# Optimization experiments

Hardware: AMD Instinct MI355X
Metric: run time of the kernel (lower is better)

## Reference

```python
import jax, jax.numpy as jnp
import numpy as np

# Graph / model dims (match init_kwargs config)
N1, N2, N3 = 80000, 16000, 4096
E1, E2 = 256000, 65536
D_IN, H1, C1 = 256, 8, 64   # conv1: concat -> 512
H2, C2 = 4, 64              # conv2: mean over heads -> gnn_outdim=64
F_IN, F_HID, L_DIM, N_CLS = 128, 64, 64, 1


def setup_inputs() -> dict:
    key = jax.random.key(0)
    ks = jax.random.split(key, 20)
    rng = np.random.default_rng(0)

    def edges(E, n_src, n_dst):
        src = rng.integers(0, n_src, size=E)
        dst = rng.integers(0, n_dst, size=E)
        # avoid incidental self loops (PyG remove_self_loops); explicit ones added in conv
        src = np.where(src == dst, src + 1, src)
        return jnp.asarray(src, jnp.int32), jnp.asarray(dst, jnp.int32)

    es1, ed1 = edges(E1, N1, N2)
    es2, ed2 = edges(E2, N2, N3)
    s = 0.05
    return {
        "x": jax.random.normal(ks[0], (N1, D_IN), jnp.float32),
        "flat": jax.random.normal(ks[1], (N3, F_IN), jnp.float32),
        "last": jax.random.normal(ks[2], (N3, L_DIM), jnp.float32),
        "edge_src1": es1, "edge_dst1": ed1,
        "edge_src2": es2, "edge_dst2": ed2,
        "W1_src": jax.random.normal(ks[3], (D_IN, H1 * C1), jnp.float32) * s,
        "W1_dst": jax.random.normal(ks[4], (D_IN, H1 * C1), jnp.float32) * s,
        "att1_src": jax.random.normal(ks[5], (H1, C1), jnp.float32) * s,
        "att1_dst": jax.random.normal(ks[6], (H1, C1), jnp.float32) * s,
        "bias1": jax.random.normal(ks[7], (H1 * C1,), jnp.float32) * s,
        "W2_src": jax.random.normal(ks[8], (H1 * C1, H2 * C2), jnp.float32) * s,
        "W2_dst": jax.random.normal(ks[9], (H1 * C1, H2 * C2), jnp.float32) * s,
        "att2_src": jax.random.normal(ks[10], (H2, C2), jnp.float32) * s,
        "att2_dst": jax.random.normal(ks[11], (H2, C2), jnp.float32) * s,
        "bias2": jax.random.normal(ks[12], (C2,), jnp.float32) * s,
        "flat_W": jax.random.normal(ks[13], (F_IN, F_HID), jnp.float32) * s,
        "flat_b": jax.random.normal(ks[14], (F_HID,), jnp.float32) * s,
        "out_W": jax.random.normal(ks[15], (C2 + F_HID + L_DIM, N_CLS), jnp.float32) * s,
        "out_b": jax.random.normal(ks[16], (N_CLS,), jnp.float32) * s,
    }


def gat_conv(x_src, x_dst, src, dst, W_s, W_d, a_s, a_d, b, concat):
    """PyG bipartite GATConv (eval mode, add_self_loops=True, neg slope 0.2)."""
    H, C = a_s.shape
    Ns, Nd = x_src.shape[0], x_dst.shape[0]
    h_s = (x_src @ W_s).reshape(Ns, H, C)
    h_d = (x_dst @ W_d).reshape(Nd, H, C)
    sl = jnp.arange(Nd, dtype=src.dtype)
    src = jnp.concatenate([src, sl])  # self loops on target nodes
    dst = jnp.concatenate([dst, sl])
    e_s = jnp.einsum("nhc,hc->nh", h_s, a_s)  # [Ns,H]
    e_d = jnp.einsum("nhc,hc->nh", h_d, a_d)  # [Nd,H]
    alpha = jax.nn.leaky_relu(e_s[src] + e_d[dst], negative_slope=0.2)  # [E,H]
    amax = jax.ops.segment_max(alpha, dst, num_segments=Nd)[dst]
    ex = jnp.exp(alpha - amax)
    w = ex / jax.ops.segment_sum(ex, dst, num_segments=Nd)[dst]  # segment softmax
    msg = w[:, :, None] * h_s[src]  # [E,H,C]
    out = jax.ops.segment_sum(msg, dst, num_segments=Nd)  # [Nd,H,C]
    out = out.reshape(Nd, H * C) if concat else out.mean(axis=1)
    return out + b


def reference(x, flat, last, edge_src1, edge_dst1, edge_src2, edge_dst2,
              W1_src, W1_dst, att1_src, att1_dst, bias1,
              W2_src, W2_dst, att2_src, att2_dst, bias2,
              flat_W, flat_b, out_W, out_b):
    # eval mode: featdrop / attndrop / main_dropout are identity
    h = gat_conv(x, x[:N2], edge_src1, edge_dst1,
                 W1_src, W1_dst, att1_src, att1_dst, bias1, concat=True)
    h = jax.nn.elu(h)
    h = gat_conv(h, h[:N3], edge_src2, edge_dst2,
                 W2_src, W2_dst, att2_src, att2_dst, bias2, concat=False)
    f = flat @ flat_W + flat_b
    z = jnp.concatenate([h, f, last], axis=1)  # [N3, 64+64+64]
    return z @ out_W + out_b  # [N3, num_cls]
```

## Files before the change

### kernel.cpp

```cpp
#include <hip/hip_runtime.h>
#include <hip/hip_bf16.h>
#include <cstdio>

typedef __attribute__((ext_vector_type(8))) short short8;
typedef __attribute__((ext_vector_type(4))) short short4v;
typedef __attribute__((ext_vector_type(8))) _Float16 half8;
typedef __attribute__((ext_vector_type(4))) float f32x4;

template <int H> struct VecT;
template <> struct VecT<8> { using T = short8; };
template <> struct VecT<4> { using T = short4v; };

__device__ __forceinline__ float bfu2f(unsigned short u) {
    return __uint_as_float(((unsigned)u) << 16);
}
__device__ __forceinline__ unsigned short f2bfu(float f) {
    __hip_bfloat16 b = __float2bfloat16(f);
    union { __hip_bfloat16 b; unsigned short u; } cv; cv.b = b;
    return cv.u;
}
__device__ __forceinline__ unsigned short f2hu(float f) {
    _Float16 h = (_Float16)f;
    union { _Float16 h; unsigned short u; } cv; cv.h = h;
    return cv.u;
}

#define N1 80000
#define N2 16000
#define N3 4096
#define E1 256000
#define E2 65536

__global__ void prep_kernel(const float* __restrict__ W1s, const float* __restrict__ W1d,
                            unsigned short* __restrict__ w1s_pk, unsigned short* __restrict__ w1d_pk,
                            const float* __restrict__ W2s, const float* __restrict__ W2d,
                            unsigned short* __restrict__ w2s_pk, unsigned short* __restrict__ w2d_pk,
                            const float* __restrict__ fW, unsigned short* __restrict__ fw_t3,
                            int* __restrict__ zbase, int zn) {
    int i = blockIdx.x * blockDim.x + threadIdx.x;
    const int S0 = 262144, S1 = 262144, S2 = 8192;
    if (i < S0) {
        const float* W = (i < 131072) ? W1s : W1d;
        unsigned short* pk = (i < 131072) ? w1s_pk : w1d_pk;
        int j = i & 131071;
        int k = j >> 9, n = j & 511;
        int n16 = n >> 4, l = n & 15, k32 = k >> 5, qq = (k >> 3) & 3, e = k & 7;
        size_t base = ((size_t)(n16 * 8 + k32)) * 512 + (qq * 16 + l) * 8 + e;
        pk[base] = f2hu(W[j]);
    } else if (i < S0 + S1) {
        int ii = i - S0;
        const float* W = (ii < 131072) ? W2s : W2d;
        unsigned short* pk = (ii < 131072) ? w2s_pk : w2d_pk;
        int j = ii & 131071;
        int k = j >> 8, n = j & 255;
        int n16 = n >> 4, l = n & 15, k32 = k >> 5, qq = (k >> 3) & 3, e = k & 7;
        size_t base = ((size_t)(n16 * 16 + k32)) * 512 + (qq * 16 + l) * 8 + e;
        pk[base] = f2hu(W[j]);
    } else if (i < S0 + S1 + S2) {
        int j = i - S0 - S1;
        int k = j >> 6, n = j & 63;
        float v = fW[j];
        unsigned short h = f2bfu(v);
        unsigned short l = f2bfu(v - bfu2f(h));
        size_t base = (size_t)n * 384;
        fw_t3[base + k] = h;
        fw_t3[base + 128 + k] = l;
        fw_t3[base + 256 + k] = h;
    } else {
        int j = i - S0 - S1 - S2;
        if (j < zn) zbase[j] = 0;
    }
}

__global__ void hist_dual(const int* __restrict__ d1, int* __restrict__ c1,
                          const int* __restrict__ d2, int* __restrict__ c2) {
    int i = blockIdx.x * blockDim.x + threadIdx.x;
    if (i < E1) {
        int d = d1[i];
        if ((unsigned)d < (unsigned)N2) atomicAdd(&c1[d], 1);
    } else if (i < E1 + E2) {
        int d = d2[i - E1];
        if ((unsigned)d < (unsigned)N3) atomicAdd(&c2[d], 1);
    }
}
__global__ __launch_bounds__(1024)
void scan_dual(const int* __restrict__ c1, int* __restrict__ s1, int Nd1,
               const int* __restrict__ c2, int* __restrict__ s2, int Nd2) {
    const int* cnt = (blockIdx.x == 0) ? c1 : c2;
    int* start = (blockIdx.x == 0) ? s1 : s2;
    int Nd = (blockIdx.x == 0) ? Nd1 : Nd2;
    __shared__ int part[1024];
    int t = threadIdx.x;
    int k = (Nd + 1023) >> 10;
    int lo = t * k, hi = min(lo + k, Nd);
    if (lo > Nd) lo = Nd;
    int s = 0;
    for (int i = lo; i < hi; i++) s += cnt[i];
    part[t] = s;
    __syncthreads();
    for (int off = 1; off < 1024; off <<= 1) {
        int v = (t >= off) ? part[t - off] : 0;
        __syncthreads();
        part[t] += v;
        __syncthreads();
    }
    int run = (t > 0) ? part[t - 1] : 0;
    for (int i = lo; i < hi; i++) { start[i] = run; run += cnt[i]; }
    if (t == 1023) start[Nd] = part[1023];
}
__global__ void fill_dual(const int* __restrict__ sa1, const int* __restrict__ da1,
                          const int* __restrict__ st1, int* __restrict__ cu1, int* __restrict__ cs1,
                          const int* __restrict__ sa2, const int* __restrict__ da2,
                          const int* __restrict__ st2, int* __restrict__ cu2, int* __restrict__ cs2) {
    int i = blockIdx.x * blockDim.x + threadIdx.x;
    const int *sa, *da, *st;
    int *cu, *cs;
    int Nd, Ns, e;
    if (i < E1) { sa = sa1; da = da1; st = st1; cu = cu1; cs = cs1; Nd = N2; Ns = N1; e = i; }
    else if (i < E1 + E2) { sa = sa2; da = da2; st = st2; cu = cu2; cs = cs2; Nd = N3; Ns = N2; e = i - E1; }
    else return;
    int d = da[e];
    if ((unsigned)d >= (unsigned)Nd) return;
    int p = atomicAdd(&cu[d], 1);
    int idx = st[d] + p;
    if (idx >= st[d + 1]) return;
    int s = sa[e];
    if ((unsigned)s >= (unsigned)Ns) s = 0;
    cs[idx] = s;
}

template <bool AF16>
__global__ __launch_bounds__(256, 2)
void gemm_lds(const void* __restrict__ Ax,
              const unsigned short* __restrict__ Bp1, unsigned short* __restrict__ C1,
              const float* __restrict__ att1, float* __restrict__ es1,
              const unsigned short* __restrict__ Bp2, unsigned short* __restrict__ C2,
              const float* __restrict__ att2, float* __restrict__ es2,
              int Mb1, int MT, int NB, int N, int K, int H) {
    __shared__ alignas(16) _Float16 As[2][64][72];
    const int hb = blockIdx.x;
    const int xcd = hb & 7;
    const int sI = hb >> 3;
    const int mt = (sI / NB) * 8 + xcd;
    const int nb = sI % NB;
    if (mt >= MT) return;
    const unsigned short* Bp; unsigned short* C; const float* att; float* es_out;
    int m0;
    if (mt < Mb1) { Bp = Bp1; C = C1; att = att1; es_out = es1; m0 = mt * 64; }
    else          { Bp = Bp2; C = C2; att = att2; es_out = es2; m0 = (mt - Mb1) * 64; }
    const int tid = threadIdx.x;
    const int wave = tid >> 6, lane = tid & 63;
    const int q = lane >> 4, l15 = lane & 15;
    const int n0 = nb * 256 + wave * 64;
    const int KS = K >> 6;
    const int KSB = K >> 5;
    const int arow = tid >> 2, ac16 = (tid & 3) * 16;
    const unsigned short* Bbase = Bp + (size_t)(n0 >> 4) * KSB * 512 + lane * 8;

    f32x4 acc[4][4] = {};
    half8 b[2][4];
    float4 s0, s1, s2, s3;
    half8 sh0, sh1;

    auto stageLoad = [&](int t) {
        if constexpr (AF16) {
            const _Float16* p = (const _Float16*)Ax + (size_t)(m0 + arow) * K + t * 64 + ac16;
            sh0 = *(const half8*)p;
            sh1 = *(const half8*)(p + 8);
        } else {
            const float* p = (const float*)Ax + (size_t)(m0 + arow) * K + t * 64 + ac16;
            s0 = *(const float4*)p;
            s1 = *(const float4*)(p + 4);
            s2 = *(const float4*)(p + 8);
            s3 = *(const float4*)(p + 12);
        }
    };
    auto stageWrite = [&](int buf) {
        half8 v0, v1;
        if constexpr (AF16) {
            v0 = sh0; v1 = sh1;
        } else {
            v0[0] = (_Float16)s0.x; v0[1] = (_Float16)s0.y;
            v0[2] = (_Float16)s0.z; v0[3] = (_Float16)s0.w;
            v0[4] = (_Float16)s1.x; v0[5] = (_Float16)s1.y;
            v0[6] = (_Float16)s1.z; v0[7] = (_Float16)s1.w;
            v1[0] = (_Float16)s2.x; v1[1] = (_Float16)s2.y;
            v1[2] = (_Float16)s2.z; v1[3] = (_Float16)s2.w;
            v1[4] = (_Float16)s3.x; v1[5] = (_Float16)s3.y;
            v1[6] = (_Float16)s3.z; v1[7] = (_Float16)s3.w;
        }
        *(half8*)&As[buf][arow][ac16] = v0;
        *(half8*)&As[buf][arow][ac16 + 8] = v1;
    };
    auto loadB = [&](int k32, int kh, int nt) {
        b[kh][nt] = *(const half8*)(Bbase + ((size_t)nt * KSB + k32) * 512);
    };

    stageLoad(0);
#pragma unroll
    for (int kh = 0; kh < 2; kh++)
#pragma unroll
        for (int nt = 0; nt < 4; nt++) loadB(kh, kh, nt);
    stageWrite(0);
    __syncthreads();

    int cur = 0;
    for (int t = 0; t < KS; t++) {
        const bool hn = (t + 1) < KS;
        if (hn) stageLoad(t + 1);
#pragma unroll
        for (int kh = 0; kh < 2; kh++) {
#pragma unroll
            for (int rg = 0; rg < 4; rg++) {
                half8 a = *(const half8*)&As[cur][rg * 16 + l15][kh * 32 + q * 8];
#pragma unroll
                for (int nt = 0; nt < 4; nt++) {
                    acc[rg][nt] = __builtin_amdgcn_mfma_f32_16x16x32_f16(a, b[kh][nt], acc[rg][nt], 0, 0, 0);
                    if (rg == 3 && hn) loadB(2 * (t + 1) + kh, kh, nt);
                }
            }
        }
        if (hn) {
            stageWrite(cur ^ 1);
            __syncthreads();
        }
        cur ^= 1;
    }

#pragma unroll
    for (int rg = 0; rg < 4; rg++)
#pragma unroll
        for (int nt = 0; nt < 4; nt++)
#pragma unroll
            for (int r = 0; r < 4; r++) {
                int row = m0 + rg * 16 + q * 4 + r;
                int col = n0 + nt * 16 + l15;
                C[(size_t)row * N + col] = f2bfu(acc[rg][nt][r]);
            }
    {
        const int head = n0 >> 6;
        float av[4];
#pragma unroll
        for (int nt = 0; nt < 4; nt++) av[nt] = att[head * 64 + nt * 16 + l15];
#pragma unroll
        for (int rg = 0; rg < 4; rg++)
#pragma unroll
            for (int r = 0; r < 4; r++) {
                float p = acc[rg][0][r] * av[0] + acc[rg][1][r] * av[1]
                        + acc[rg][2][r] * av[2] + acc[rg][3][r] * av[3];
#pragma unroll
                for (int off = 1; off < 16; off <<= 1) p += __shfl_xor(p, off);
                if (l15 == 0)
                    es_out[(size_t)(m0 + rg * 16 + q * 4 + r) * H + head] = p;
            }
    }
}

__global__ __launch_bounds__(256)
void gemm_mfma(const float* __restrict__ A, const unsigned short* __restrict__ Bt3,
               float* __restrict__ C, int M, int N, int K) {
    const int KK = 3 * K;
    __shared__ unsigned short As[2][64][72];
    __shared__ unsigned short Bs[64][72];
    const int tid = threadIdx.x;
    const int wave = tid >> 6, lane = tid & 63;
    const int wr = wave >> 1, wc = wave & 1;
    const int quad = lane >> 4, l15 = lane & 15;
    const int m0 = blockIdx.y * 64, n0 = blockIdx.x * 64;
    f32x4 acc[2][2] = {};
    for (int k0 = 0; k0 < KK; k0 += 64) {
        const int seg = k0 / K;
        const int ks = k0 - seg * K;
#pragma unroll
        for (int i = 0; i < 2; i++) {
            int idx = tid + i * 256;
            int r = idx >> 3, cv = (idx & 7) * 8;
            const float* ap = &A[(size_t)(m0 + r) * K + ks + cv];
            const float4 v0 = *(const float4*)ap;
            const float4 v1 = *(const float4*)(ap + 4);
            float va[8] = {v0.x, v0.y, v0.z, v0.w, v1.x, v1.y, v1.z, v1.w};
            short8 h8, l8;
#pragma unroll
            for (int j = 0; j < 8; j++) {
                unsigned short hh = f2bfu(va[j]);
                h8[j] = (short)hh;
                l8[j] = (short)f2bfu(va[j] - bfu2f(hh));
            }
            *(short8*)&As[0][r][cv] = h8;
            *(short8*)&As[1][r][cv] = l8;
            *(short8*)&Bs[r][cv] = *(const short8*)&Bt3[(size_t)(n0 + r) * KK + k0 + cv];
        }
        __syncthreads();
        const int abank = (seg < 2) ? 0 : 1;
#pragma unroll
        for (int kk = 0; kk < 64; kk += 32) {
            short8 a[2], b[2];
#pragma unroll
            for (int t = 0; t < 2; t++) {
                a[t] = *(const short8*)&As[abank][wr * 32 + t * 16 + l15][kk + quad * 8];
                b[t] = *(const short8*)&Bs[wc * 32 + t * 16 + l15][kk + quad * 8];
            }
#pragma unroll
            for (int mt = 0; mt < 2; mt++)
#pragma unroll
                for (int nt = 0; nt < 2; nt++)
                    acc[mt][nt] = __builtin_amdgcn_mfma_f32_16x16x32_bf16(
                        a[mt], b[nt], acc[mt][nt], 0, 0, 0);
        }
        __syncthreads();
    }
#pragma unroll
    for (int mt = 0; mt < 2; mt++)
#pragma unroll
        for (int nt = 0; nt < 2; nt++)
#pragma unroll
            for (int r = 0; r < 4; r++) {
                int row = m0 + wr * 32 + mt * 16 + quad * 4 + r;
                int col = n0 + wc * 32 + nt * 16 + l15;
                C[(size_t)row * N + col] = acc[mt][nt][r];
            }
}

template <int H, bool ELU, bool HOUT>
__global__ __launch_bounds__(256)
void gat_agg2(const int* __restrict__ csr, const int* __restrict__ rs,
              const unsigned short* __restrict__ hs,
              const float* __restrict__ es,
              const float* __restrict__ ed,
              const float* __restrict__ bias,
              void* __restrict__ out,
              int Nd) {
    constexpr int LH = (H == 8) ? 3 : 2;
    constexpr int EPC = 64 >> LH;
    const int lane = threadIdx.x & 63;
    const int d = blockIdx.x * (blockDim.x >> 6) + (threadIdx.x >> 6);
    if (d >= Nd) return;
    const int beg = rs[d];
    const int deg = rs[d + 1] - beg;
    const int n = deg + 1;
    const int h = lane & (H - 1);
    const int e0 = lane >> LH;
    const float edh = ed[(size_t)d * H + h];
    const int nch = (n + EPC - 1) / EPC;
    float mx = -1e30f;
    float den = 0.0f;
    if (nch <= 8) {
        float ac[8];
#pragma unroll
        for (int c = 0; c < 8; c++) {
            float a = -1e30f;
            if (c < nch) {
                int j = c * EPC + e0;
                if (j < n) {
                    int s = (j < deg) ? csr[beg + j] : d;
                    a = es[(size_t)s * H + h] + edh;
                    a = (a > 0.0f) ? a : 0.2f * a;
                }
            }
            ac[c] = a;
            mx = fmaxf(mx, a);
        }
#pragma unroll
        for (int off = H; off < 64; off <<= 1) mx = fmaxf(mx, __shfl_xor(mx, off));
#pragma unroll
        for (int c = 0; c < 8; c++)
            if (c < nch) den += expf(ac[c] - mx);
#pragma unroll
        for (int off = H; off < 64; off <<= 1) den += __shfl_xor(den, off);
    } else {
        for (int j0 = 0; j0 < n; j0 += EPC) {
            int j = j0 + e0;
            if (j < n) {
                int s = (j < deg) ? csr[beg + j] : d;
                float a = es[(size_t)s * H + h] + edh;
                a = (a > 0.0f) ? a : 0.2f * a;
                mx = fmaxf(mx, a);
            }
        }
#pragma unroll
        for (int off = H; off < 64; off <<= 1) mx = fmaxf(mx, __shfl_xor(mx, off));
        for (int j0 = 0; j0 < n; j0 += EPC) {
            int j = j0 + e0;
            if (j < n) {
                int s = (j < deg) ? csr[beg + j] : d;
                float a = es[(size_t)s * H + h] + edh;
                a = (a > 0.0f) ? a : 0.2f * a;
                den += expf(a - mx);
            }
        }
#pragma unroll
        for (int off = H; off < 64; off <<= 1) den += __shfl_xor(den, off);
    }
    const float inv = 1.0f / den;
    const int hB = lane >> (6 - LH);
    const float mB = __shfl(mx, hB);
    const float invB = __shfl(inv, hB);
    const float edhB = __shfl(edh, hB);
    using V = typename VecT<H>::T;
    float acc[H] = {};
    const size_t rowoff = (size_t)lane * H;
    int j = 0;
    for (; j + 8 <= n; j += 8) {
        int s[8]; V rv[8]; float w[8];
#pragma unroll
        for (int u = 0; u < 8; u++) { int jj = j + u; s[u] = (jj < deg) ? csr[beg + jj] : d; }
#pragma unroll
        for (int u = 0; u < 8; u++) rv[u] = *(const V*)&hs[(size_t)s[u] * (H * 64) + rowoff];
#pragma unroll
        for (int u = 0; u < 8; u++) {
            float a = es[(size_t)s[u] * H + hB] + edhB;
            a = (a > 0.0f) ? a : 0.2f * a;
            w[u] = expf(a - mB) * invB;
        }
#pragma unroll
        for (int u = 0; u < 8; u++)
#pragma unroll
            for (int k = 0; k < H; k++) acc[k] += w[u] * bfu2f((unsigned short)rv[u][k]);
    }
    for (; j + 4 <= n; j += 4) {
        int s[4]; V rv[4]; float w[4];
#pragma unroll
        for (int u = 0; u < 4; u++) { int jj = j + u; s[u] = (jj < deg) ? csr[beg + jj] : d; }
#pragma unroll
        for (int u = 0; u < 4; u++) rv[u] = *(const V*)&hs[(size_t)s[u] * (H * 64) + rowoff];
#pragma unroll
        for (int u = 0; u < 4; u++) {
            float a = es[(size_t)s[u] * H + hB] + edhB;
            a = (a > 0.0f) ? a : 0.2f * a;
            w[u] = expf(a - mB) * invB;
        }
#pragma unroll
        for (int u = 0; u < 4; u++)
#pragma unroll
            for (int k = 0; k < H; k++) acc[k] += w[u] * bfu2f((unsigned short)rv[u][k]);
    }
    for (; j < n; j++) {
        int s = (j < deg) ? csr[beg + j] : d;
        V rv = *(const V*)&hs[(size_t)s * (H * 64) + rowoff];
        float a = es[(size_t)s * H + hB] + edhB;
        a = (a > 0.0f) ? a : 0.2f * a;
        float w = expf(a - mB) * invB;
#pragma unroll
        for (int k = 0; k < H; k++) acc[k] += w * bfu2f((unsigned short)rv[k]);
    }
#pragma unroll
    for (int k = 0; k < H; k++) {
        float v = acc[k];
        if (ELU) {
            v += bias[lane * H + k];
            v = (v > 0.0f) ? v : expm1f(v);
        }
        acc[k] = v;
    }
    if constexpr (HOUT) {
        half8 hv;
#pragma unroll
        for (int k = 0; k < H; k++) hv[k] = (_Float16)acc[k];
        _Float16* op = (_Float16*)out + (size_t)d * (H * 64) + rowoff;
        *(half8*)op = hv;
    } else {
        float* op = (float*)out + (size_t)d * (H * 64) + rowoff;
#pragma unroll
        for (int qd = 0; qd < H / 4; qd++)
            *(float4*)&op[qd * 4] = *(float4*)&acc[qd * 4];
    }
}

__global__ void final_kernel(const float* __restrict__ acc2, const float* __restrict__ bias2,
                             const float* __restrict__ fbuf, const float* __restrict__ flat_b,
                             const float* __restrict__ last, const float* __restrict__ outW,
                             const float* __restrict__ outb, float* __restrict__ out, int N) {
    int n = blockIdx.x * blockDim.x + threadIdx.x;
    if (n >= N) return;
    float s = outb[0];
    const float* a = acc2 + (size_t)n * 256;
    for (int c = 0; c < 64; c++) {
        float h2 = 0.25f * (a[c] + a[64 + c] + a[128 + c] + a[192 + c]) + bias2[c];
        s += h2 * outW[c];
        s += (fbuf[(size_t)n * 64 + c] + flat_b[c]) * outW[64 + c];
        s += last[(size_t)n * 64 + c] * outW[128 + c];
    }
    out[n] = s;
}

extern "C" void kernel_launch(void* const* d_in, const int* in_sizes, int n_in,
                              void* d_out, int out_size, void* d_ws, size_t ws_size,
                              hipStream_t stream) {
    const float* x    = (const float*)d_in[0];
    const float* flat = (const float*)d_in[1];
    const float* last = (const float*)d_in[2];
    const int*  es1i  = (const int*)d_in[3];
    const int*  ed1i  = (const int*)d_in[4];
    const int*  es2i  = (const int*)d_in[5];
    const int*  ed2i  = (const int*)d_in[6];
    const float* W1s  = (const float*)d_in[7];
    const float* W1d  = (const float*)d_in[8];
    const float* a1s  = (const float*)d_in[9];
    const float* a1d  = (const float*)d_in[10];
    const float* b1   = (const float*)d_in[11];
    const float* W2s  = (const float*)d_in[12];
    const float* W2d  = (const float*)d_in[13];
    const float* a2s  = (const float*)d_in[14];
    const float* a2d  = (const float*)d_in[15];
    const float* b2   = (const float*)d_in[16];
    const float* fW   = (const float*)d_in[17];
    const float* fb   = (const float*)d_in[18];
    const float* oW   = (const float*)d_in[19];
    const float* ob   = (const float*)d_in[20];
    float* out = (float*)d_out;

    float* ws = (float*)d_ws;
    unsigned short* hs1_bf = (unsigned short*)ws;
    unsigned short* hd1_bf = (unsigned short*)(ws + 20480000);
    float* es1f = ws + 24576000;
    float* ed1f = ws + 25216000;
    float* acc1 = ws + 25344000;
    unsigned short* wb = (unsigned short*)(ws + 54016000);
    unsigned short* w1s_pk = wb;
    unsigned short* w1d_pk = wb + 262144;
    unsigned short* w2s_pk = wb + 524288;
    unsigned short* w2d_pk = wb + 786432;
    unsigned short* fw_t3  = wb + 1048576;
    int* ibase   = (int*)(ws + 54816000);
    int* cnt1    = ibase;
    int* cursor1 = ibase + 16000;
    int* cnt2    = ibase + 32000;
    int* cursor2 = ibase + 36096;
    int* start1  = ibase + 40192;
    int* start2  = ibase + 56193;
    int* csr1    = ibase + 60290;
    int* csr2    = ibase + 316290;
    const size_t NEED = ((size_t)54816000 + 381826) * 4;
    if (ws_size < NEED) {
        fprintf(stderr, "kernel_launch: ws_size %zu < needed %zu\n", ws_size, NEED);
        return;
    }
    unsigned short* hs2_bf = (unsigned short*)ws;
    unsigned short* hd2_bf = (unsigned short*)(ws + 2048000);
    float* es2f = ws + 2572288;
    float* ed2f = ws + 2636288;
    float* acc2 = ws + 2652672;
    float* fbuf = ws + 3701248;
    unsigned short* acc1h = (unsigned short*)acc1;

    {
        int total = 262144 + 262144 + 8192 + 40192;
        prep_kernel<<<(total + 255) / 256, 256, 0, stream>>>(
            W1s, W1d, w1s_pk, w1d_pk,
            W2s, W2d, w2s_pk, w2d_pk,
            fW, fw_t3, ibase, 40192);
    }
    hist_dual<<<(E1 + E2 + 255) / 256, 256, 0, stream>>>(ed1i, cnt1, ed2i, cnt2);
    scan_dual<<<2, 1024, 0, stream>>>(cnt1, start1, N2, cnt2, start2, N3);
    fill_dual<<<(E1 + E2 + 255) / 256, 256, 0, stream>>>(
        es1i, ed1i, start1, cursor1, csr1, es2i, ed2i, start2, cursor2, csr2);

    {
        const int MT = N1 / 64 + N2 / 64;
        const int NB = 512 / 256;
        const int grid = 8 * NB * ((MT + 7) / 8);
        gemm_lds<false><<<grid, 256, 0, stream>>>(
            x, w1s_pk, hs1_bf, a1s, es1f,
            w1d_pk, hd1_bf, a1d, ed1f,
            N1 / 64, MT, NB, 512, 256, 8);
    }
    gat_agg2<8, true, true><<<N2 / 4, 256, 0, stream>>>(
        csr1, start1, hs1_bf, es1f, ed1f, b1, acc1h, N2);

    {
        const int MT = N2 / 64 + N3 / 64;
        const int NB = 1;
        const int grid = 8 * NB * ((MT + 7) / 8);
        gemm_lds<true><<<grid, 256, 0, stream>>>(
            acc1h, w2s_pk, hs2_bf, a2s, es2f,
            w2d_pk, hd2_bf, a2d, ed2f,
            N2 / 64, MT, NB, 256, 512, 4);
    }
    gat_agg2<4, false, false><<<N3 / 4, 256, 0, stream>>>(
        csr2, start2, hs2_bf, es2f, ed2f, nullptr, acc2, N3);

    gemm_mfma<<<dim3(1, N3 / 64), 256, 0, stream>>>(flat, fw_t3, fbuf, N3, 64, 128);
    final_kernel<<<(N3 + 255) / 256, 256, 0, stream>>>(acc2, b2, fbuf, fb, last, oW, ob, out, N3);
}
```

Before: 379.2 us.

## Fold destination attention into precomputed W_dst·a_dst vectors, drop dst GEMMs

The destination-side projection GEMM is no longer computed. Its only use was the attention logit e_d, so W_dst·att_dst is precomputed per head in the prep kernel and e_d is taken as a dot product of the raw destination features inside the aggregation kernel. This removes the N2 and N3 dst tiles from both GEMM launches and the hd buffers. The aggregation kernel also now reuses the cached per-chunk softmax exponentials in the low-degree path instead of recomputing es lookups and exp per edge. The cost is extra per-node dot-product work in aggregation and a small serial loop in prep, plus a reassociation of the fp math for e_d.

```diff
diff --git a/kernel.cpp b/kernel.cpp
--- a/kernel.cpp
+++ b/kernel.cpp
@@ -31,31 +31,27 @@
 #define E1 256000
 #define E2 65536
 
-__global__ void prep_kernel(const float* __restrict__ W1s, const float* __restrict__ W1d,
-                            unsigned short* __restrict__ w1s_pk, unsigned short* __restrict__ w1d_pk,
-                            const float* __restrict__ W2s, const float* __restrict__ W2d,
-                            unsigned short* __restrict__ w2s_pk, unsigned short* __restrict__ w2d_pk,
+__global__ void prep_kernel(const float* __restrict__ W1s, unsigned short* __restrict__ w1s_pk,
+                            const float* __restrict__ W2s, unsigned short* __restrict__ w2s_pk,
+                            const float* __restrict__ W1d, const float* __restrict__ a1d,
+                            float* __restrict__ v1dT,
+                            const float* __restrict__ W2d, const float* __restrict__ a2d,
+                            float* __restrict__ v2dT,
                             const float* __restrict__ fW, unsigned short* __restrict__ fw_t3,
                             int* __restrict__ zbase, int zn) {
     int i = blockIdx.x * blockDim.x + threadIdx.x;
-    const int S0 = 262144, S1 = 262144, S2 = 8192;
+    const int S0 = 131072, S1 = 131072, S2 = 8192, S3 = 4096;
     if (i < S0) {
-        const float* W = (i < 131072) ? W1s : W1d;
-        unsigned short* pk = (i < 131072) ? w1s_pk : w1d_pk;
-        int j = i & 131071;
-        int k = j >> 9, n = j & 511;
+        int k = i >> 9, n = i & 511;
         int n16 = n >> 4, l = n & 15, k32 = k >> 5, qq = (k >> 3) & 3, e = k & 7;
         size_t base = ((size_t)(n16 * 8 + k32)) * 512 + (qq * 16 + l) * 8 + e;
-        pk[base] = f2hu(W[j]);
+        w1s_pk[base] = f2hu(W1s[i]);
     } else if (i < S0 + S1) {
-        int ii = i - S0;
-        const float* W = (ii < 131072) ? W2s : W2d;
-        unsigned short* pk = (ii < 131072) ? w2s_pk : w2d_pk;
-        int j = ii & 131071;
+        int j = i - S0;
         int k = j >> 8, n = j & 255;
         int n16 = n >> 4, l = n & 15, k32 = k >> 5, qq = (k >> 3) & 3, e = k & 7;
         size_t base = ((size_t)(n16 * 16 + k32)) * 512 + (qq * 16 + l) * 8 + e;
-        pk[base] = f2hu(W[j]);
+        w2s_pk[base] = f2hu(W2s[j]);
     } else if (i < S0 + S1 + S2) {
         int j = i - S0 - S1;
         int k = j >> 6, n = j & 63;
@@ -66,8 +62,22 @@
         fw_t3[base + k] = h;
         fw_t3[base + 128 + k] = l;
         fw_t3[base + 256 + k] = h;
+    } else if (i < S0 + S1 + S2 + S3) {
+        int j = i - S0 - S1 - S2;
+        if (j < 2048) {
+            int h = j >> 8, k = j & 255;
+            float s = 0.f;
+            for (int c = 0; c < 64; c++) s += W1d[k * 512 + h * 64 + c] * a1d[h * 64 + c];
+            v1dT[j] = s;
+        } else {
+            int jj = j - 2048;
+            int h = jj >> 9, k = jj & 511;
+            float s = 0.f;
+            for (int c = 0; c < 64; c++) s += W2d[k * 256 + h * 64 + c] * a2d[h * 64 + c];
+            v2dT[jj] = s;
+        }
     } else {
-        int j = i - S0 - S1 - S2;
+        int j = i - S0 - S1 - S2 - S3;
         if (j < zn) zbase[j] = 0;
     }
 }
@@ -132,11 +142,9 @@
 template <bool AF16>
 __global__ __launch_bounds__(256, 2)
 void gemm_lds(const void* __restrict__ Ax,
-              const unsigned short* __restrict__ Bp1, unsigned short* __restrict__ C1,
-              const float* __restrict__ att1, float* __restrict__ es1,
-              const unsigned short* __restrict__ Bp2, unsigned short* __restrict__ C2,
-              const float* __restrict__ att2, float* __restrict__ es2,
-              int Mb1, int MT, int NB, int N, int K, int H) {
+              const unsigned short* __restrict__ Bp, unsigned short* __restrict__ C,
+              const float* __restrict__ att, float* __restrict__ es_out,
+              int MT, int NB, int N, int K, int H) {
     __shared__ alignas(16) _Float16 As[2][64][72];
     const int hb = blockIdx.x;
     const int xcd = hb & 7;
@@ -144,10 +152,7 @@
     const int mt = (sI / NB) * 8 + xcd;
     const int nb = sI % NB;
     if (mt >= MT) return;
-    const unsigned short* Bp; unsigned short* C; const float* att; float* es_out;
-    int m0;
-    if (mt < Mb1) { Bp = Bp1; C = C1; att = att1; es_out = es1; m0 = mt * 64; }
-    else          { Bp = Bp2; C = C2; att = att2; es_out = es2; m0 = (mt - Mb1) * 64; }
+    const int m0 = mt * 64;
     const int tid = threadIdx.x;
     const int wave = tid >> 6, lane = tid & 63;
     const int q = lane >> 4, l15 = lane & 15;
@@ -321,31 +326,58 @@
             }
 }
 
-template <int H, bool ELU, bool HOUT>
+template <int H, bool ELU, bool HOUT, bool XF16, int KD>
 __global__ __launch_bounds__(256)
 void gat_agg2(const int* __restrict__ csr, const int* __restrict__ rs,
               const unsigned short* __restrict__ hs,
               const float* __restrict__ es,
-              const float* __restrict__ ed,
+              const void* __restrict__ xsrc,
+              const float* __restrict__ vdT,
               const float* __restrict__ bias,
               void* __restrict__ out,
               int Nd) {
     constexpr int LH = (H == 8) ? 3 : 2;
     constexpr int EPC = 64 >> LH;
+    constexpr int KPL = KD / EPC;
     const int lane = threadIdx.x & 63;
     const int d = blockIdx.x * (blockDim.x >> 6) + (threadIdx.x >> 6);
     if (d >= Nd) return;
+    const int h = lane & (H - 1);
+    const int e0 = lane >> LH;
+    float edh = 0.f;
+    {
+        const float* vp = vdT + h * KD + e0 * KPL;
+        if constexpr (XF16) {
+            const _Float16* xr = (const _Float16*)xsrc + (size_t)d * KD + e0 * KPL;
+#pragma unroll
+            for (int i8 = 0; i8 < KPL / 8; i8++) {
+                half8 hx = *(const half8*)(xr + i8 * 8);
+#pragma unroll
+                for (int jj = 0; jj < 8; jj++) edh += (float)hx[jj] * vp[i8 * 8 + jj];
+            }
+        } else {
+            const float* xr = (const float*)xsrc + (size_t)d * KD + e0 * KPL;
+#pragma unroll
+            for (int i4 = 0; i4 < KPL / 4; i4++) {
+                float4 xv = *(const float4*)(xr + i4 * 4);
+                float4 vv = *(const float4*)(vp + i4 * 4);
+                edh += xv.x * vv.x + xv.y * vv.y + xv.z * vv.z + xv.w * vv.w;
+            }
+        }
+#pragma unroll
+        for (int off = H; off < 64; off <<= 1) edh += __shfl_xor(edh, off);
+    }
     const int beg = rs[d];
     const int deg = rs[d + 1] - beg;
     const int n = deg + 1;
-    const int h = lane & (H - 1);
-    const int e0 = lane >> LH;
-    const float edh = ed[(size_t)d * H + h];
     const int nch = (n + EPC - 1) / EPC;
-    float mx = -1e30f;
-    float den = 0.0f;
+    const int hB = lane >> (6 - LH);
+    using V = typename VecT<H>::T;
+    float acc[H] = {};
+    const size_t rowoff = (size_t)lane * H;
     if (nch <= 8) {
         float ac[8];
+        float mx = -1e30f;
 #pragma unroll
         for (int c = 0; c < 8; c++) {
             float a = -1e30f;
@@ -362,12 +394,38 @@
         }
 #pragma unroll
         for (int off = H; off < 64; off <<= 1) mx = fmaxf(mx, __shfl_xor(mx, off));
+        float den = 0.0f;
 #pragma unroll
         for (int c = 0; c < 8; c++)
             if (c < nch) den += expf(ac[c] - mx);
 #pragma unroll
         for (int off = H; off < 64; off <<= 1) den += __shfl_xor(den, off);
+        const float inv = 1.0f / den;
+        float ec[8];
+#pragma unroll
+        for (int c = 0; c < 8; c++) ec[c] = expf(ac[c] - mx) * inv;
+#pragma unroll
+        for (int c = 0; c < 8; c++) {
+            if (c >= nch) break;
+            const int jb = c * EPC;
+            const int cnt = min(EPC, n - jb);
+            int s[EPC]; V rv[EPC];
+#pragma unroll
+            for (int u = 0; u < EPC; u++)
+                if (u < cnt) { int jj = jb + u; s[u] = (jj < deg) ? csr[beg + jj] : d; }
+#pragma unroll
+            for (int u = 0; u < EPC; u++)
+                if (u < cnt) rv[u] = *(const V*)&hs[(size_t)s[u] * (H * 64) + rowoff];
+#pragma unroll
+            for (int u = 0; u < EPC; u++)
+                if (u < cnt) {
+                    float w = __shfl(ec[c], u * H + hB);
+#pragma unroll
+                    for (int k = 0; k < H; k++) acc[k] += w * bfu2f((unsigned short)rv[u][k]);
+                }
+        }
     } else {
+        float mx = -1e30f;
         for (int j0 = 0; j0 < n; j0 += EPC) {
             int j = j0 + e0;
             if (j < n) {
@@ -379,6 +437,7 @@
         }
 #pragma unroll
         for (int off = H; off < 64; off <<= 1) mx = fmaxf(mx, __shfl_xor(mx, off));
+        float den = 0.0f;
         for (int j0 = 0; j0 < n; j0 += EPC) {
             int j = j0 + e0;
             if (j < n) {
@@ -390,58 +449,37 @@
         }
 #pragma unroll
         for (int off = H; off < 64; off <<= 1) den += __shfl_xor(den, off);
-    }
-    const float inv = 1.0f / den;
-    const int hB = lane >> (6 - LH);
-    const float mB = __shfl(mx, hB);
-    const float invB = __shfl(inv, hB);
-    const float edhB = __shfl(edh, hB);
-    using V = typename VecT<H>::T;
-    float acc[H] = {};
-    const size_t rowoff = (size_t)lane * H;
-    int j = 0;
-    for (; j + 8 <= n; j += 8) {
-        int s[8]; V rv[8]; float w[8];
-#pragma unroll
-        for (int u = 0; u < 8; u++) { int jj = j + u; s[u] = (jj < deg) ? csr[beg + jj] : d; }
-#pragma unroll
-        for (int u = 0; u < 8; u++) rv[u] = *(const V*)&hs[(size_t)s[u] * (H * 64) + rowoff];
-#pragma unroll
-        for (int u = 0; u < 8; u++) {
-            float a = es[(size_t)s[u] * H + hB] + edhB;
+        const float inv = 1.0f / den;
+        const float mB = __shfl(mx, hB);
+        const float invB = __shfl(inv, hB);
+        const float edhB = __shfl(edh, hB);
+        int j = 0;
+        for (; j + 4 <= n; j += 4) {
+            int s[4]; V rv[4]; float w[4];
+#pragma unroll
+            for (int u = 0; u < 4; u++) { int jj = j + u; s[u] = (jj < deg) ? csr[beg + jj] : d; }
+#pragma unroll
+            for (int u = 0; u < 4; u++) rv[u] = *(const V*)&hs[(size_t)s[u] * (H * 64) + rowoff];
+#pragma unroll
+            for (int u = 0; u < 4; u++) {
+                float a = es[(size_t)s[u] * H + hB] + edhB;
+                a = (a > 0.0f) ? a : 0.2f * a;
+                w[u] = expf(a - mB) * invB;
+            }
+#pragma unroll
+            for (int u = 0; u < 4; u++)
+#pragma unroll
+                for (int k = 0; k < H; k++) acc[k] += w[u] * bfu2f((unsigned short)rv[u][k]);
+        }
+        for (; j < n; j++) {
+            int s = (j < deg) ? csr[beg + j] : d;
+            V rv = *(const V*)&hs[(size_t)s * (H * 64) + rowoff];
+            float a = es[(size_t)s * H + hB] + edhB;
             a = (a > 0.0f) ? a : 0.2f * a;
-            w[u] = expf(a - mB) * invB;
-        }
-#pragma unroll
-        for (int u = 0; u < 8; u++)
-#pragma unroll
-            for (int k = 0; k < H; k++) acc[k] += w[u] * bfu2f((unsigned short)rv[u][k]);
-    }
-    for (; j + 4 <= n; j += 4) {
-        int s[4]; V rv[4]; float w[4];
-#pragma unroll
-        for (int u = 0; u < 4; u++) { int jj = j + u; s[u] = (jj < deg) ? csr[beg + jj] : d; }
-#pragma unroll
-        for (int u = 0; u < 4; u++) rv[u] = *(const V*)&hs[(size_t)s[u] * (H * 64) + rowoff];
-#pragma unroll
-        for (int u = 0; u < 4; u++) {
-            float a = es[(size_t)s[u] * H + hB] + edhB;
-            a = (a > 0.0f) ? a : 0.2f * a;
-            w[u] = expf(a - mB) * invB;
-        }
-#pragma unroll
-        for (int u = 0; u < 4; u++)
-#pragma unroll
-            for (int k = 0; k < H; k++) acc[k] += w[u] * bfu2f((unsigned short)rv[u][k]);
-    }
-    for (; j < n; j++) {
-        int s = (j < deg) ? csr[beg + j] : d;
-        V rv = *(const V*)&hs[(size_t)s * (H * 64) + rowoff];
-        float a = es[(size_t)s * H + hB] + edhB;
-        a = (a > 0.0f) ? a : 0.2f * a;
-        float w = expf(a - mB) * invB;
-#pragma unroll
-        for (int k = 0; k < H; k++) acc[k] += w * bfu2f((unsigned short)rv[k]);
+            float w = expf(a - mB) * invB;
+#pragma unroll
+            for (int k = 0; k < H; k++) acc[k] += w * bfu2f((unsigned short)rv[k]);
+        }
     }
 #pragma unroll
     for (int k = 0; k < H; k++) {
@@ -511,16 +549,14 @@
 
     float* ws = (float*)d_ws;
     unsigned short* hs1_bf = (unsigned short*)ws;
-    unsigned short* hd1_bf = (unsigned short*)(ws + 20480000);
     float* es1f = ws + 24576000;
-    float* ed1f = ws + 25216000;
     float* acc1 = ws + 25344000;
     unsigned short* wb = (unsigned short*)(ws + 54016000);
     unsigned short* w1s_pk = wb;
-    unsigned short* w1d_pk = wb + 262144;
     unsigned short* w2s_pk = wb + 524288;
-    unsigned short* w2d_pk = wb + 786432;
     unsigned short* fw_t3  = wb + 1048576;
+    float* v1dT = ws + 54600000;
+    float* v2dT = ws + 54602048;
     int* ibase   = (int*)(ws + 54816000);
     int* cnt1    = ibase;
     int* cursor1 = ibase + 16000;
@@ -536,18 +572,16 @@
         return;
     }
     unsigned short* hs2_bf = (unsigned short*)ws;
-    unsigned short* hd2_bf = (unsigned short*)(ws + 2048000);
     float* es2f = ws + 2572288;
-    float* ed2f = ws + 2636288;
     float* acc2 = ws + 2652672;
     float* fbuf = ws + 3701248;
     unsigned short* acc1h = (unsigned short*)acc1;
 
     {
-        int total = 262144 + 262144 + 8192 + 40192;
+        int total = 131072 + 131072 + 8192 + 4096 + 40192;
         prep_kernel<<<(total + 255) / 256, 256, 0, stream>>>(
-            W1s, W1d, w1s_pk, w1d_pk,
-            W2s, W2d, w2s_pk, w2d_pk,
+            W1s, w1s_pk, W2s, w2s_pk,
+            W1d, a1d, v1dT, W2d, a2d, v2dT,
             fW, fw_t3, ibase, 40192);
     }
     hist_dual<<<(E1 + E2 + 255) / 256, 256, 0, stream>>>(ed1i, cnt1, ed2i, cnt2);
@@ -556,28 +590,23 @@
         es1i, ed1i, start1, cursor1, csr1, es2i, ed2i, start2, cursor2, csr2);
 
     {
-        const int MT = N1 / 64 + N2 / 64;
-        const int NB = 512 / 256;
+        const int MT = N1 / 64;
+        const int NB = 2;
         const int grid = 8 * NB * ((MT + 7) / 8);
         gemm_lds<false><<<grid, 256, 0, stream>>>(
-            x, w1s_pk, hs1_bf, a1s, es1f,
-            w1d_pk, hd1_bf, a1d, ed1f,
-            N1 / 64, MT, NB, 512, 256, 8);
-    }
-    gat_agg2<8, true, true><<<N2 / 4, 256, 0, stream>>>(
-        csr1, start1, hs1_bf, es1f, ed1f, b1, acc1h, N2);
+            x, w1s_pk, hs1_bf, a1s, es1f, MT, NB, 512, 256, 8);
+    }
+    gat_agg2<8, true, true, false, 256><<<N2 / 4, 256, 0, stream>>>(
+        csr1, start1, hs1_bf, es1f, x, v1dT, b1, acc1h, N2);
 
     {
-        const int MT = N2 / 64 + N3 / 64;
-        const int NB = 1;
-        const int grid = 8 * NB * ((MT + 7) / 8);
+        const int MT = N2 / 64;
+        const int grid = 8 * ((MT + 7) / 8);
         gemm_lds<true><<<grid, 256, 0, stream>>>(
-            acc1h, w2s_pk, hs2_bf, a2s, es2f,
-            w2d_pk, hd2_bf, a2d, ed2f,
-            N2 / 64, MT, NB, 256, 512, 4);
-    }
-    gat_agg2<4, false, false><<<N3 / 4, 256, 0, stream>>>(
-        csr2, start2, hs2_bf, es2f, ed2f, nullptr, acc2, N3);
+            acc1h, w2s_pk, hs2_bf, a2s, es2f, MT, 1, 256, 512, 4);
+    }
+    gat_agg2<4, false, false, true, 512><<<N3 / 4, 256, 0, stream>>>(
+        csr2, start2, hs2_bf, es2f, acc1h, v2dT, nullptr, acc2, N3);
 
     gemm_mfma<<<dim3(1, N3 / 64), 256, 0, stream>>>(flat, fw_t3, fbuf, N3, 64, 128);
     final_kernel<<<(N3 + 255) / 256, 256, 0, stream>>>(acc2, b2, fbuf, fb, last, oW, ob, out, N3);
```

Result: no change. 385.0 us (+1.5%).
